# Performance work log

Hardware: AMD Instinct MI355X
Metric: run time of the kernel (lower is better)

## Reference

```python
import jax, jax.numpy as jnp
import numpy as np

IM_SIZE = (256, 256)
GRID_SIZE = (512, 512)
J = 6                    # numpoints per dim
L = 1024                 # table oversampling
ALPHA = 2.34 * J         # Kaiser-Bessel alpha (order 0)
CENTER = J * L // 2      # center index of the KB table
B, C, M = 2, 16, 409600  # batch, coils, k-space points


def _kb_ft(f, J_, alpha):
    """Fourier transform of the order-0 Kaiser-Bessel kernel (Fessler)."""
    z = np.sqrt((np.pi * J_ * f) ** 2 - alpha ** 2 + 0j)
    z = np.where(np.abs(z) < 1e-12, 1e-12, z)
    return np.real(J_ * np.sinh(z) / (z * np.i0(alpha)))


def _build_table(J_, L_, K, N, alpha):
    """Oversampled KB kernel table with the linear phase that centers the
    apodization at (N-1)/2 (torchkbnufft stores complex tables for this reason)."""
    u = (np.arange(J_ * L_ + 1) - J_ * L_ / 2.0) / L_  # grid-unit offsets in [-J/2, J/2]
    fr = np.sqrt(np.maximum(0.0, 1.0 - (2.0 * u / J_) ** 2))
    kb = np.where(np.abs(u) <= J_ / 2.0, np.i0(alpha * fr) / np.i0(alpha), 0.0)
    tab = kb * np.exp(-1j * (2.0 * np.pi / K) * u * (N - 1) / 2.0)
    return np.stack([tab.real, tab.imag]).astype(np.float32)


def setup_inputs():
    key = jax.random.key(0)
    k1, k2 = jax.random.split(key)
    x = jax.random.normal(k1, (B, C, 2) + IM_SIZE, dtype=jnp.float32)
    om = jax.random.uniform(k2, (B, 2, M), dtype=jnp.float32, minval=-jnp.pi, maxval=jnp.pi)
    scs = []
    for d in range(2):
        n = np.arange(IM_SIZE[d]) - (IM_SIZE[d] - 1) / 2.0
        scs.append(1.0 / _kb_ft(n / GRID_SIZE[d], J, ALPHA))
    sc = np.outer(scs[0], scs[1])
    scaling_coef = jnp.asarray(np.stack([sc, np.zeros_like(sc)]).astype(np.float32))
    table_0 = jnp.asarray(_build_table(J, L, GRID_SIZE[0], IM_SIZE[0], ALPHA))
    table_1 = jnp.asarray(_build_table(J, L, GRID_SIZE[1], IM_SIZE[1], ALPHA))
    n_shift = jnp.asarray(np.array([IM_SIZE[0] // 2, IM_SIZE[1] // 2], dtype=np.float32))
    return {"x": x, "om": om, "scaling_coef": scaling_coef,
            "table_0": table_0, "table_1": table_1, "n_shift": n_shift}


def reference(x, om, scaling_coef, table_0, table_1, n_shift):
    K0, K1 = GRID_SIZE
    # apodize by scaling coefficients, zero-pad to the oversampled grid, FFT
    xc = (x[:, :, 0] + 1j * x[:, :, 1]) * (scaling_coef[0] + 1j * scaling_coef[1])
    xc = jnp.pad(xc, ((0, 0), (0, 0), (0, K0 - IM_SIZE[0]), (0, K1 - IM_SIZE[1])))
    Gf = jnp.fft.fftn(xc, axes=(-2, -1)).reshape(xc.shape[0], xc.shape[1], K0 * K1)
    t0 = table_0[0] + 1j * table_0[1]
    t1 = table_1[0] + 1j * table_1[1]
    # fractional grid coordinates of the off-grid points
    tm0 = om[:, 0] * (K0 / (2.0 * jnp.pi))  # (B, M)
    tm1 = om[:, 1] * (K1 / (2.0 * jnp.pi))
    koff0 = jnp.floor(tm0 - J / 2.0).astype(jnp.int32) + 1
    koff1 = jnp.floor(tm1 - J / 2.0).astype(jnp.int32) + 1
    # per-dim table-lookup coefficients and wrapped grid indices
    c0, i0, c1, i1 = [], [], [], []
    for j in range(J):
        g0 = koff0 + j
        g1 = koff1 + j
        c0.append(t0[jnp.round((tm0 - g0) * L).astype(jnp.int32) + CENTER])
        c1.append(t1[jnp.round((tm1 - g1) * L).astype(jnp.int32) + CENTER])
        i0.append(jnp.mod(g0, K0))
        i1.append(jnp.mod(g1, K1))
    # separable J x J neighbor accumulation (matches Jlist loop in torchkbnufft)
    kdat = jnp.zeros((Gf.shape[0], Gf.shape[1], tm0.shape[-1]), dtype=Gf.dtype)
    for a in range(J):
        for b in range(J):
            idx = (i0[a] * K1 + i1[b])[:, None, :]          # (B, 1, M)
            vals = jnp.take_along_axis(Gf, idx, axis=2)     # (B, C, M) gather
            kdat = kdat + (c0[a] * c1[b])[:, None, :] * vals
    # fftshift phase
    phase = jnp.exp(1j * (om[:, 0] * n_shift[0] + om[:, 1] * n_shift[1]))
    kdat = kdat * phase[:, None, :]
    return jnp.stack([kdat.real, kdat.imag], axis=2)  # (B, C, 2, M)
```

## Files before the change

kernel.cpp:

```cpp
#include <hip/hip_runtime.h>
#include <math.h>

#define BB 2
#define CC 16
#define MM 409600
#define NI 256
#define JJ 6
#define TABLE_LEN 6145
#define CENTER 3072
#define TILE 32
#define TDIM 16
#define NTILES 256
#define HALO 38
#define NBINS 512
#define CAP 2048
#define BINC_STRIDE 16
#define SC_PPB 4096
#define SC_THREADS 1024
#define SC_PPT 4
#define GRP 4

__global__ void fft512_row_fused(const float* __restrict__ x, const float* __restrict__ sc,
                                 float2* __restrict__ gf, int b) {
  __shared__ float2 bufA[512];
  __shared__ float2 bufB[512];
  int line = blockIdx.x;
  int c = line >> 9;
  int gi = line & 511;
  int t = threadIdx.x;
  float2* g = gf + (size_t)line * 512;
  if (gi >= NI) {
    g[t] = make_float2(0.f, 0.f);
    g[t + 256] = make_float2(0.f, 0.f);
    return;
  }
  const float* xb = x + (size_t)(b * CC + c) * 2 * NI * NI + gi * NI;
  float xr = xb[t];
  float xi = xb[NI * NI + t];
  const float* scb = sc + gi * NI;
  float sr = scb[t];
  float si = scb[NI * NI + t];
  bufA[t] = make_float2(xr * sr - xi * si, xr * si + xi * sr);
  bufA[t + 256] = make_float2(0.f, 0.f);
  __syncthreads();
  float2* X = bufA;
  float2* Y = bufB;
  const float C0 = -6.283185307179586f / 512.0f;
  #pragma unroll
  for (int k = 0; k < 9; ++k) {
    int s = 1 << k;
    float2 a = X[t];
    float2 bb = X[t + 256];
    int ps = t & ~(s - 1);
    float ang = C0 * (float)ps;
    float wr, wi;
    __sincosf(ang, &wi, &wr);
    int wbase = ((t >> k) << (k + 1)) | (t & (s - 1));
    float2 dif = make_float2(a.x - bb.x, a.y - bb.y);
    Y[wbase] = make_float2(a.x + bb.x, a.y + bb.y);
    Y[wbase + s] = make_float2(dif.x * wr - dif.y * wi, dif.x * wi + dif.y * wr);
    __syncthreads();
    float2* tmp = X; X = Y; Y = tmp;
  }
  g[t] = X[t];
  g[t + 256] = X[t + 256];
}

__global__ void fft512_col(float2* __restrict__ data) {
  __shared__ float2 bufA[512 * 8];
  __shared__ float2 bufB[512 * 8];
  int blk = blockIdx.x;
  int img = blk >> 6;
  int cg = blk & 63;
  float2* g = data + ((size_t)img << 18) + cg * 8;
  int t = threadIdx.x;
  int col = t & 7;
  int r0 = t >> 3;
  #pragma unroll
  for (int k = 0; k < 4; ++k) {
    int row = r0 + 128 * k;
    bufA[row * 8 + col] = g[(size_t)row * 512 + col];
  }
  __syncthreads();
  float2* X = bufA;
  float2* Y = bufB;
  const float C0 = -6.283185307179586f / 512.0f;
  #pragma unroll
  for (int k = 0; k < 9; ++k) {
    int s = 1 << k;
    #pragma unroll
    for (int h = 0; h < 2; ++h) {
      int j = r0 + 128 * h;
      float2 a = X[j * 8 + col];
      float2 b = X[(j + 256) * 8 + col];
      int ps = j & ~(s - 1);
      float ang = C0 * (float)ps;
      float wr, wi;
      __sincosf(ang, &wi, &wr);
      int wbase = ((j >> k) << (k + 1)) | (j & (s - 1));
      float2 dif = make_float2(a.x - b.x, a.y - b.y);
      Y[wbase * 8 + col] = make_float2(a.x + b.x, a.y + b.y);
      Y[(wbase + s) * 8 + col] = make_float2(dif.x * wr - dif.y * wi, dif.x * wi + dif.y * wr);
    }
    __syncthreads();
    float2* tmp = X; X = Y; Y = tmp;
  }
  #pragma unroll
  for (int k = 0; k < 4; ++k) {
    int row = r0 + 128 * k;
    g[(size_t)row * 512 + col] = X[row * 8 + col];
  }
}

__global__ void zero_bins(int* __restrict__ binc) {
  int t = blockIdx.x * blockDim.x + threadIdx.x;
  if (t < NBINS * BINC_STRIDE) binc[t] = 0;
}

__global__ void scatter_points(const float* __restrict__ om,
                               int* __restrict__ binc,
                               float2* __restrict__ bpts, int* __restrict__ invcap) {
  __shared__ int lhist[NBINS];
  __shared__ int lbase[NBINS];
  __shared__ int lpos[NBINS];
  int t = threadIdx.x;
  int bid = blockIdx.x;
  if (t < NBINS) { lhist[t] = 0; lpos[t] = 0; }
  __syncthreads();
  const float scale = 81.48733086305042f;
  float ptm0[SC_PPT], ptm1[SC_PPT];
  int pbin[SC_PPT];
  #pragma unroll
  for (int i = 0; i < SC_PPT; ++i) {
    int idx = bid * SC_PPB + i * SC_THREADS + t;
    int b = idx / MM;
    int m = idx - b * MM;
    float om0 = om[(size_t)b * 2 * MM + m];
    float om1 = om[(size_t)b * 2 * MM + MM + m];
    float tm0 = om0 * scale;
    float tm1 = om1 * scale;
    int s0 = ((int)floorf(tm0 - 3.0f) + 1) & 511;
    int s1 = ((int)floorf(tm1 - 3.0f) + 1) & 511;
    int bin = b * NTILES + (s0 >> 5) * TDIM + (s1 >> 5);
    ptm0[i] = tm0; ptm1[i] = tm1;
    pbin[i] = bin;
    atomicAdd(&lhist[bin], 1);
  }
  __syncthreads();
  if (t < NBINS) lbase[t] = atomicAdd(&binc[t * BINC_STRIDE], lhist[t]);
  __syncthreads();
  #pragma unroll
  for (int i = 0; i < SC_PPT; ++i) {
    int idx = bid * SC_PPB + i * SC_THREADS + t;
    int bin = pbin[i];
    int pos = atomicAdd(&lpos[bin], 1);
    int slot = lbase[bin] + pos;
    if (slot < CAP) {
      bpts[bin * CAP + slot] = make_float2(ptm0[i], ptm1[i]);
    }
    int sl = slot < CAP ? slot : CAP - 1;
    invcap[idx] = (bin << 11) | sl;
  }
}

__global__ void prefix_bins(const int* __restrict__ binc, int* __restrict__ dbase) {
  __shared__ int buf[NBINS];
  int t = threadIdx.x;
  int c = binc[t * BINC_STRIDE];
  c = c < 0 ? 0 : (c > CAP ? CAP : c);
  buf[t] = c;
  __syncthreads();
  int seg = t & (NTILES - 1);
  for (int off = 1; off < NTILES; off <<= 1) {
    int val = (seg >= off) ? buf[t - off] : 0;
    __syncthreads();
    buf[t] += val;
    __syncthreads();
  }
  dbase[t] = buf[t] - c;
}

__global__ void __launch_bounds__(256, 4)
interp_binned(const float2* __restrict__ gf,
              const float2* __restrict__ bpts,
              const int* __restrict__ binc,
              const int* __restrict__ dbase,
              const float* __restrict__ t0,
              const float* __restrict__ t1,
              float2* __restrict__ tmp, int b) {
  __shared__ float2 lds[GRP * HALO * HALO];
  int blk = blockIdx.x;
  int grp = blk & (CC / GRP - 1);
  int tile = blk >> 2;
  int cbase = grp * GRP;
  int tile0 = tile >> 4, tile1 = tile & 15;
  int base0 = tile0 * TILE, base1 = tile1 * TILE;
  int tid = threadIdx.x;
  for (int i = tid; i < GRP * HALO * HALO; i += 256) {
    int cc = i / (HALO * HALO);
    int rem = i - cc * (HALO * HALO);
    int r = rem / HALO;
    int cl = rem - r * HALO;
    const float2* img = gf + ((size_t)(cbase + cc) << 18);
    lds[i] = img[(((base0 + r) & 511) << 9) | ((base1 + cl) & 511)];
  }
  __syncthreads();
  int bin = b * NTILES + tile;
  int count = binc[bin * BINC_STRIDE];
  count = count < 0 ? 0 : (count > CAP ? CAP : count);
  int pbase = bin * CAP;
  int dbin = dbase[bin];
  for (int p = tid; p < count; p += 256) {
    float2 pt = bpts[pbase + p];
    float tm0 = pt.x, tm1 = pt.y;
    int koff0 = (int)floorf(tm0 - 3.0f) + 1;
    int koff1 = (int)floorf(tm1 - 3.0f) + 1;
    int d0 = ((koff0 & 511) - base0) & 31;
    int d1 = ((koff1 & 511) - base1) & 31;
    float c0r[JJ], c0i[JJ], c1r[JJ], c1i[JJ];
    #pragma unroll
    for (int j = 0; j < JJ; ++j) {
      int idx0 = (int)rintf((tm0 - (float)(koff0 + j)) * 1024.0f) + CENTER;
      idx0 = idx0 < 0 ? 0 : (idx0 > TABLE_LEN - 1 ? TABLE_LEN - 1 : idx0);
      c0r[j] = t0[idx0];
      c0i[j] = t0[TABLE_LEN + idx0];
      int idx1 = (int)rintf((tm1 - (float)(koff1 + j)) * 1024.0f) + CENTER;
      idx1 = idx1 < 0 ? 0 : (idx1 > TABLE_LEN - 1 ? TABLE_LEN - 1 : idx1);
      c1r[j] = t1[idx1];
      c1i[j] = t1[TABLE_LEN + idx1];
    }
    float2 res[GRP];
    #pragma unroll
    for (int g = 0; g < GRP; ++g) {
      const float2* hal = lds + g * (HALO * HALO);
      float ar = 0.f, ai = 0.f;
      #pragma unroll
      for (int ja = 0; ja < JJ; ++ja) {
        const float2* row = hal + (d0 + ja) * HALO + d1;
        float rr = 0.f, ri = 0.f;
        #pragma unroll
        for (int jb = 0; jb < JJ; ++jb) {
          float2 v = row[jb];
          rr += c1r[jb] * v.x - c1i[jb] * v.y;
          ri += c1r[jb] * v.y + c1i[jb] * v.x;
        }
        ar += c0r[ja] * rr - c0i[ja] * ri;
        ai += c0r[ja] * ri + c0i[ja] * rr;
      }
      res[g] = make_float2(ar, ai);
    }
    float4* d4 = (float4*)(tmp + (size_t)(dbin + p) * CC + cbase);
    d4[0] = make_float4(res[0].x, res[0].y, res[1].x, res[1].y);
    d4[1] = make_float4(res[2].x, res[2].y, res[3].x, res[3].y);
  }
}

__global__ void gather_out(const float2* __restrict__ tmp, const int* __restrict__ invcap,
                           const int* __restrict__ dbase, const float* __restrict__ om,
                           const float* __restrict__ nshift, float* __restrict__ out, int b) {
  int m = blockIdx.x * blockDim.x + threadIdx.x;
  if (m >= MM) return;
  int v = invcap[b * MM + m];
  int bin = v >> 11;
  int pos = v & (CAP - 1);
  int slot = dbase[bin] + pos;
  float om0 = om[(size_t)b * 2 * MM + m];
  float om1 = om[(size_t)b * 2 * MM + MM + m];
  float ph = om0 * nshift[0] + om1 * nshift[1];
  float sp, cp;
  sincosf(ph, &sp, &cp);
  const float4* src = (const float4*)(tmp + (size_t)slot * CC);
  float* ob = out + (size_t)b * CC * 2 * MM + m;
  #pragma unroll
  for (int k = 0; k < 8; ++k) {
    float4 v4 = src[k];
    float r0 = v4.x * cp - v4.y * sp;
    float i0 = v4.x * sp + v4.y * cp;
    float r1 = v4.z * cp - v4.w * sp;
    float i1 = v4.z * sp + v4.w * cp;
    int c = 2 * k;
    ob[(size_t)(2 * c) * MM] = r0;
    ob[(size_t)(2 * c + 1) * MM] = i0;
    ob[(size_t)(2 * c + 2) * MM] = r1;
    ob[(size_t)(2 * c + 3) * MM] = i1;
  }
}

extern "C" void kernel_launch(void* const* d_in, const int* in_sizes, int n_in,
                              void* d_out, int out_size, void* d_ws, size_t ws_size,
                              hipStream_t stream) {
  const float* x = (const float*)d_in[0];
  const float* om = (const float*)d_in[1];
  const float* sc = (const float*)d_in[2];
  const float* t0 = (const float*)d_in[3];
  const float* t1 = (const float*)d_in[4];
  const float* nshift = (const float*)d_in[5];
  float* out = (float*)d_out;

  char* ws = (char*)d_ws;
  float2* gf = (float2*)ws;
  size_t off = (size_t)CC * 512 * 512 * sizeof(float2);
  float2* bpts = (float2*)(ws + off); off += (size_t)NBINS * CAP * sizeof(float2);
  float2* tmp = (float2*)(ws + off);  off += (size_t)MM * CC * sizeof(float2);
  int* invcap = (int*)(ws + off);     off += (size_t)BB * MM * sizeof(int);
  int* binc = (int*)(ws + off);       off += (size_t)NBINS * BINC_STRIDE * sizeof(int);
  int* dbase = (int*)(ws + off);      off += (size_t)NBINS * sizeof(int);

  zero_bins<<<(NBINS * BINC_STRIDE + 255) / 256, 256, 0, stream>>>(binc);
  scatter_points<<<BB * MM / SC_PPB, SC_THREADS, 0, stream>>>(om, binc, bpts, invcap);
  prefix_bins<<<1, NBINS, 0, stream>>>(binc, dbase);
  for (int b = 0; b < BB; ++b) {
    fft512_row_fused<<<CC * 512, 256, 0, stream>>>(x, sc, gf, b);
    fft512_col<<<CC * 64, 1024, 0, stream>>>(gf);
    interp_binned<<<NTILES * (CC / GRP), 256, 0, stream>>>(gf, bpts, binc, dbase, t0, t1, tmp, b);
    gather_out<<<MM / 256, 256, 0, stream>>>(tmp, invcap, dbase, om, nshift, out, b);
  }
}
```

Baseline: 501.3 us.

## Sort points within bins by cell and store interp output grouped by coil group

Adds a per-bin counting sort that reorders binned k-space points by their 6x6 stencil origin cell and records a permutation, so neighbouring threads in interp_binned read nearby LDS halo entries and run more uniform work. The tmp buffer layout changes from point-major over 16 coils to coil-group-major, so each interp block writes contiguous 32-byte chunks and gather_out reads from four planes. The cost is an extra sort kernel, a permutation lookup in gather_out, and scattered rewrites of bpts.

```diff
diff --git a/kernel.cpp b/kernel.cpp
--- a/kernel.cpp
+++ b/kernel.cpp
@@ -19,6 +19,8 @@
 #define SC_THREADS 1024
 #define SC_PPT 4
 #define GRP 4
+#define SB_THREADS 256
+#define SB_PPT 8
 
 __global__ void fft512_row_fused(const float* __restrict__ x, const float* __restrict__ sc,
                                  float2* __restrict__ gf, int b) {
@@ -178,6 +180,59 @@
     __syncthreads();
   }
   dbase[t] = buf[t] - c;
+}
+
+__global__ void sort_bins(float2* __restrict__ bpts, const int* __restrict__ binc,
+                          unsigned short* __restrict__ perm) {
+  __shared__ int hist[1024];
+  __shared__ int part[SB_THREADS];
+  int bin = blockIdx.x;
+  int t = threadIdx.x;
+  int n = binc[bin * BINC_STRIDE];
+  n = n < 0 ? 0 : (n > CAP ? CAP : n);
+  for (int i = t; i < 1024; i += SB_THREADS) hist[i] = 0;
+  __syncthreads();
+  float2 pts[SB_PPT];
+  int keys[SB_PPT];
+  #pragma unroll
+  for (int i = 0; i < SB_PPT; ++i) {
+    int p = t + i * SB_THREADS;
+    keys[i] = -1;
+    if (p < n) {
+      float2 pt = bpts[bin * CAP + p];
+      int d0 = (((int)floorf(pt.x - 3.0f)) + 1) & 31;
+      int d1 = (((int)floorf(pt.y - 3.0f)) + 1) & 31;
+      keys[i] = (d0 << 5) | d1;
+      pts[i] = pt;
+      atomicAdd(&hist[keys[i]], 1);
+    }
+  }
+  __syncthreads();
+  int base = 4 * t;
+  int h0 = hist[base], h1 = hist[base + 1], h2 = hist[base + 2], h3 = hist[base + 3];
+  int sum = h0 + h1 + h2 + h3;
+  part[t] = sum;
+  __syncthreads();
+  for (int off = 1; off < SB_THREADS; off <<= 1) {
+    int v = (t >= off) ? part[t - off] : 0;
+    __syncthreads();
+    part[t] += v;
+    __syncthreads();
+  }
+  int excl = part[t] - sum;
+  hist[base] = excl;
+  hist[base + 1] = excl + h0;
+  hist[base + 2] = excl + h0 + h1;
+  hist[base + 3] = excl + h0 + h1 + h2;
+  __syncthreads();
+  #pragma unroll
+  for (int i = 0; i < SB_PPT; ++i) {
+    if (keys[i] >= 0) {
+      int np = atomicAdd(&hist[keys[i]], 1);
+      bpts[bin * CAP + np] = pts[i];
+      perm[bin * CAP + (t + i * SB_THREADS)] = (unsigned short)np;
+    }
+  }
 }
 
 __global__ void __launch_bounds__(256, 4)
@@ -249,40 +304,42 @@
       }
       res[g] = make_float2(ar, ai);
     }
-    float4* d4 = (float4*)(tmp + (size_t)(dbin + p) * CC + cbase);
+    float4* d4 = (float4*)(tmp + ((size_t)grp * MM + dbin + p) * GRP);
     d4[0] = make_float4(res[0].x, res[0].y, res[1].x, res[1].y);
     d4[1] = make_float4(res[2].x, res[2].y, res[3].x, res[3].y);
   }
 }
 
 __global__ void gather_out(const float2* __restrict__ tmp, const int* __restrict__ invcap,
-                           const int* __restrict__ dbase, const float* __restrict__ om,
+                           const int* __restrict__ dbase, const unsigned short* __restrict__ perm,
+                           const float* __restrict__ om,
                            const float* __restrict__ nshift, float* __restrict__ out, int b) {
   int m = blockIdx.x * blockDim.x + threadIdx.x;
   if (m >= MM) return;
   int v = invcap[b * MM + m];
   int bin = v >> 11;
   int pos = v & (CAP - 1);
-  int slot = dbase[bin] + pos;
+  int slot = dbase[bin] + (int)perm[bin * CAP + pos];
   float om0 = om[(size_t)b * 2 * MM + m];
   float om1 = om[(size_t)b * 2 * MM + MM + m];
   float ph = om0 * nshift[0] + om1 * nshift[1];
   float sp, cp;
   sincosf(ph, &sp, &cp);
-  const float4* src = (const float4*)(tmp + (size_t)slot * CC);
   float* ob = out + (size_t)b * CC * 2 * MM + m;
   #pragma unroll
-  for (int k = 0; k < 8; ++k) {
-    float4 v4 = src[k];
-    float r0 = v4.x * cp - v4.y * sp;
-    float i0 = v4.x * sp + v4.y * cp;
-    float r1 = v4.z * cp - v4.w * sp;
-    float i1 = v4.z * sp + v4.w * cp;
-    int c = 2 * k;
-    ob[(size_t)(2 * c) * MM] = r0;
-    ob[(size_t)(2 * c + 1) * MM] = i0;
-    ob[(size_t)(2 * c + 2) * MM] = r1;
-    ob[(size_t)(2 * c + 3) * MM] = i1;
+  for (int g = 0; g < 4; ++g) {
+    const float4* src = (const float4*)(tmp + ((size_t)g * MM + slot) * GRP);
+    float4 v0 = src[0];
+    float4 v1 = src[1];
+    int c = 4 * g;
+    ob[(size_t)(2 * c + 0) * MM] = v0.x * cp - v0.y * sp;
+    ob[(size_t)(2 * c + 1) * MM] = v0.x * sp + v0.y * cp;
+    ob[(size_t)(2 * c + 2) * MM] = v0.z * cp - v0.w * sp;
+    ob[(size_t)(2 * c + 3) * MM] = v0.z * sp + v0.w * cp;
+    ob[(size_t)(2 * c + 4) * MM] = v1.x * cp - v1.y * sp;
+    ob[(size_t)(2 * c + 5) * MM] = v1.x * sp + v1.y * cp;
+    ob[(size_t)(2 * c + 6) * MM] = v1.z * cp - v1.w * sp;
+    ob[(size_t)(2 * c + 7) * MM] = v1.z * sp + v1.w * cp;
   }
 }
 
@@ -303,16 +360,18 @@
   float2* bpts = (float2*)(ws + off); off += (size_t)NBINS * CAP * sizeof(float2);
   float2* tmp = (float2*)(ws + off);  off += (size_t)MM * CC * sizeof(float2);
   int* invcap = (int*)(ws + off);     off += (size_t)BB * MM * sizeof(int);
+  unsigned short* perm = (unsigned short*)(ws + off); off += (size_t)NBINS * CAP * sizeof(unsigned short);
   int* binc = (int*)(ws + off);       off += (size_t)NBINS * BINC_STRIDE * sizeof(int);
   int* dbase = (int*)(ws + off);      off += (size_t)NBINS * sizeof(int);
 
   zero_bins<<<(NBINS * BINC_STRIDE + 255) / 256, 256, 0, stream>>>(binc);
   scatter_points<<<BB * MM / SC_PPB, SC_THREADS, 0, stream>>>(om, binc, bpts, invcap);
   prefix_bins<<<1, NBINS, 0, stream>>>(binc, dbase);
+  sort_bins<<<NBINS, SB_THREADS, 0, stream>>>(bpts, binc, perm);
   for (int b = 0; b < BB; ++b) {
     fft512_row_fused<<<CC * 512, 256, 0, stream>>>(x, sc, gf, b);
     fft512_col<<<CC * 64, 1024, 0, stream>>>(gf);
     interp_binned<<<NTILES * (CC / GRP), 256, 0, stream>>>(gf, bpts, binc, dbase, t0, t1, tmp, b);
-    gather_out<<<MM / 256, 256, 0, stream>>>(tmp, invcap, dbase, om, nshift, out, b);
-  }
-}
+    gather_out<<<MM / 256, 256, 0, stream>>>(tmp, invcap, dbase, perm, om, nshift, out, b);
+  }
+}
```

Result: no change. 504.0 us (+0.6%).
